# Performance work log

Measured on AMD Instinct MI355X. Metric: run time of the kernel, lower is better.

## Reference

```python
import jax, jax.numpy as jnp
import numpy as np

N_NODES = 100000
N_EDGES = 300000
D_IN = 256
D_OUT = 256
NEG_SLOPE = 0.2


def setup_inputs() -> dict:
    key = jax.random.key(0)
    ks = jax.random.split(key, 6)
    feat = jax.random.normal(ks[0], (N_NODES, D_IN), dtype=jnp.float32)
    # xavier-normal-ish init scale
    scale = (2.0 / (D_IN + D_OUT)) ** 0.5
    W_src = jax.random.normal(ks[1], (D_IN, D_OUT), dtype=jnp.float32) * scale
    b_src = jnp.zeros((D_OUT,), dtype=jnp.float32)
    W_dst = jax.random.normal(ks[2], (D_IN, D_OUT), dtype=jnp.float32) * scale
    b_dst = jnp.zeros((D_OUT,), dtype=jnp.float32)
    attn = jax.random.normal(ks[3], (D_OUT,), dtype=jnp.float32) * scale
    src = jax.random.randint(ks[4], (N_EDGES,), 0, N_NODES, dtype=jnp.int32)
    dst = jax.random.randint(ks[5], (N_EDGES,), 0, N_NODES, dtype=jnp.int32)
    return {"feat": feat, "W_src": W_src, "b_src": b_src,
            "W_dst": W_dst, "b_dst": b_dst, "attn": attn,
            "src": src, "dst": dst}


def reference(feat, W_src, b_src, W_dst, b_dst, attn, src, dst):
    N = feat.shape[0]
    # node projections (dense GEMMs)
    el = feat @ W_src + b_src          # [N, D_OUT]  (feat_src / 'el')
    er = feat @ W_dst + b_dst          # [N, D_OUT]  (feat_dst / 'er')
    # edge-wise u_add_v + LeakyReLU, then attention dot
    e = jax.nn.leaky_relu(el[src] + er[dst], NEG_SLOPE)  # [E, D_OUT]
    score = e @ attn                    # [E]  ((e*attn).sum(-1))
    # edge softmax segmented by destination node
    smax = jax.ops.segment_max(score, dst, num_segments=N)   # [N]
    ex = jnp.exp(score - smax[dst])                           # [E]
    ssum = jax.ops.segment_sum(ex, dst, num_segments=N)      # [N]
    a = ex / ssum[dst]                                        # [E]
    # weighted scatter-sum aggregation: u_mul_e('el','a') -> sum per dst
    out = jax.ops.segment_sum(el[src] * a[:, None], dst, num_segments=N)
    return out  # [N, D_OUT]
```

## Files before the change

kernel.cpp:

```cpp
#include <hip/hip_runtime.h>
#include <cstdint>
#include <cmath>

#define D 256
#define NEG 0.2f
#define BK 64

typedef __attribute__((ext_vector_type(8))) __bf16 bf16x8;
typedef __attribute__((ext_vector_type(8))) unsigned short ushort8;
typedef __attribute__((ext_vector_type(4))) float f32x4;

__device__ __forceinline__ unsigned short f2bf(float f){
    unsigned u = __float_as_uint(f);
    return (unsigned short)((u + 0x7fffu + ((u >> 16) & 1u)) >> 16);
}
__device__ __forceinline__ float b2f(unsigned short u){
    return __uint_as_float(((unsigned)u) << 16);
}

__device__ __forceinline__ void gload_lds16(const void* g, void* l){
    __builtin_amdgcn_global_load_lds(
        (const __attribute__((address_space(1))) unsigned int*)g,
        (__attribute__((address_space(3))) unsigned int*)l, 16, 0, 0);
}

__global__ __launch_bounds__(256) void prep_w_kernel(
    const float* __restrict__ Wsrc, const float* __restrict__ Wdst,
    const float* __restrict__ bsrc, const float* __restrict__ bdst,
    unsigned short* __restrict__ WT, float* __restrict__ biascat)
{
    int idx = blockIdx.x*256 + threadIdx.x;
    int col = idx >> 5;
    int u   = idx & 31;
    int gu  = (u & 24) | ((u ^ col) & 7);
    const float* W = (col < 256) ? Wsrc : Wdst;
    int c = col & 255;
    ushort8 o;
    #pragma unroll
    for (int j = 0; j < 8; ++j)
        o[j] = f2bf(W[(size_t)(gu*8 + j)*D + c]);
    *(ushort8*)(WT + (size_t)col*D + u*8) = o;
    if (idx < 512) biascat[idx] = (idx < 256) ? bsrc[idx] : bdst[idx-256];
}

__global__ __launch_bounds__(256) void prep_feat_kernel(
    const float* __restrict__ feat, unsigned short* __restrict__ featb, int N, int NPAD)
{
    int total = NPAD * 32;
    for (int idx = blockIdx.x*256 + threadIdx.x; idx < total; idx += gridDim.x*256){
        int r = idx >> 5;
        int u = idx & 31;
        ushort8 o;
        if (r < N){
            int gu = (u & 24) | ((u ^ r) & 7);
            const float* s = feat + (size_t)r*D + gu*8;
            float4 a = *(const float4*)s;
            float4 b = *(const float4*)(s + 4);
            o[0]=f2bf(a.x); o[1]=f2bf(a.y); o[2]=f2bf(a.z); o[3]=f2bf(a.w);
            o[4]=f2bf(b.x); o[5]=f2bf(b.y); o[6]=f2bf(b.z); o[7]=f2bf(b.w);
        } else {
            #pragma unroll
            for (int j = 0; j < 8; ++j) o[j] = 0;
        }
        *(ushort8*)(featb + (size_t)r*D + u*8) = o;
    }
}

__global__ __launch_bounds__(256) void proj_mfma_kernel(
    const unsigned short* __restrict__ featb, const unsigned short* __restrict__ WT,
    const float* __restrict__ biascat,
    unsigned short* __restrict__ el16, unsigned short* __restrict__ er16, int N)
{
    __shared__ unsigned short As[128*BK];
    __shared__ unsigned short Bs[128*BK];

    const int tid  = threadIdx.x;
    const int wave = tid >> 6;
    const int lane = tid & 63;
    const int col0 = blockIdx.x * 128;
    const int row0 = blockIdx.y * 128;
    const int wr = (wave >> 1) * 64;
    const int wc = (wave & 1) * 64;
    const int l15 = lane & 15;
    const int kg  = lane >> 4;

    const int sr = (wave << 3) + (lane >> 3);
    const int sc = (lane & 7) * 8;

    f32x4 acc[4][4] = {};

    for (int k0 = 0; k0 < D; k0 += BK) {
        #pragma unroll
        for (int r4 = 0; r4 < 4; ++r4) {
            int ar = r4*32 + sr;
            gload_lds16(featb + (size_t)(row0 + ar)*D + k0 + sc,
                        &As[(r4*32 + wave*8)*BK]);
            gload_lds16(WT + (size_t)(col0 + ar)*D + k0 + sc,
                        &Bs[(r4*32 + wave*8)*BK]);
        }
        __syncthreads();

        #pragma unroll
        for (int ks = 0; ks < 2; ++ks) {
            bf16x8 af[4], bfr[4];
            #pragma unroll
            for (int m = 0; m < 4; ++m){
                int row = wr + m*16 + l15;
                int c = ((kg + ks*4) ^ (row & 7)) * 8;
                af[m] = *(const bf16x8*)&As[row*BK + c];
            }
            #pragma unroll
            for (int n = 0; n < 4; ++n){
                int row = wc + n*16 + l15;
                int c = ((kg + ks*4) ^ (row & 7)) * 8;
                bfr[n] = *(const bf16x8*)&Bs[row*BK + c];
            }
            #pragma unroll
            for (int m = 0; m < 4; ++m)
                #pragma unroll
                for (int n = 0; n < 4; ++n)
                    acc[m][n] = __builtin_amdgcn_mfma_f32_16x16x32_bf16(bfr[n], af[m], acc[m][n], 0, 0, 0);
        }
        __syncthreads();
    }

    unsigned short* __restrict__ dstp = (col0 < 256) ? el16 : er16;
    const int ccbase = col0 & 255;
    #pragma unroll
    for (int m = 0; m < 4; ++m) {
        int row = row0 + wr + m*16 + l15;
        if (row >= N) continue;
        #pragma unroll
        for (int n = 0; n < 4; ++n) {
            int cw = wc + n*16 + kg*4;
            float4 b4 = *(const float4*)(biascat + col0 + cw);
            ushort4 o;
            o.x = f2bf(acc[m][n][0] + b4.x);
            o.y = f2bf(acc[m][n][1] + b4.y);
            o.z = f2bf(acc[m][n][2] + b4.z);
            o.w = f2bf(acc[m][n][3] + b4.w);
            *(ushort4*)(dstp + (size_t)row*D + ccbase + cw) = o;
        }
    }
}

__global__ void count_kernel(const int* __restrict__ dst, int* __restrict__ deg, int E){
    int e = blockIdx.x*blockDim.x + threadIdx.x;
    if (e < E) atomicAdd(&deg[dst[e]], 1);
}

__global__ __launch_bounds__(256) void scan1_kernel(const int* __restrict__ deg,
                                                    int* __restrict__ incl,
                                                    int* __restrict__ bsum, int N){
    __shared__ int s[256];
    int i = blockIdx.x*256 + threadIdx.x;
    int v = (i < N) ? deg[i] : 0;
    s[threadIdx.x] = v;
    __syncthreads();
    #pragma unroll
    for (int off = 1; off < 256; off <<= 1){
        int t = (threadIdx.x >= off) ? s[threadIdx.x - off] : 0;
        __syncthreads();
        s[threadIdx.x] += t;
        __syncthreads();
    }
    if (i < N) incl[i] = s[threadIdx.x];
    if (threadIdx.x == 255) bsum[blockIdx.x] = s[255];
}

__global__ __launch_bounds__(512) void scan2_kernel(int* __restrict__ bsum, int nb){
    __shared__ int s[512];
    int t = threadIdx.x;
    int v = (t < nb) ? bsum[t] : 0;
    s[t] = v;
    __syncthreads();
    #pragma unroll
    for (int off = 1; off < 512; off <<= 1){
        int u = (t >= off) ? s[t - off] : 0;
        __syncthreads();
        s[t] += u;
        __syncthreads();
    }
    if (t < nb) bsum[t] = s[t] - v;
}

__global__ __launch_bounds__(256) void scan3_kernel(const int* __restrict__ deg,
                                                    const int* __restrict__ incl,
                                                    const int* __restrict__ bsum,
                                                    int* __restrict__ rowstart,
                                                    int* __restrict__ cursor, int N){
    int i = blockIdx.x*256 + threadIdx.x;
    if (i < N){
        int st = incl[i] - deg[i] + bsum[blockIdx.x];
        rowstart[i] = st;
        cursor[i]   = st;
    }
}

__global__ void scatter_kernel(const int* __restrict__ dst, const int* __restrict__ src,
                               int* __restrict__ cursor, int* __restrict__ srcs, int E){
    int e = blockIdx.x*blockDim.x + threadIdx.x;
    if (e < E){
        int pos = atomicAdd(&cursor[dst[e]], 1);
        srcs[pos] = src[e];
    }
}

__global__ __launch_bounds__(256) void gat_node_kernel(
    const unsigned short* __restrict__ el16, const unsigned short* __restrict__ er16,
    const float* __restrict__ attn, const int* __restrict__ srcs,
    const int* __restrict__ rowstart, const int* __restrict__ degv,
    float* __restrict__ out, int N)
{
    int node = blockIdx.x*4 + (threadIdx.x >> 6);
    if (node >= N) return;
    int lane = threadIdx.x & 63;
    float4 o = make_float4(0.f,0.f,0.f,0.f);
    int deg = degv[node];
    float* op = out + (size_t)node*D + lane*4;
    if (deg == 0){ *(float4*)op = o; return; }

    ushort4 rv = *(const ushort4*)(er16 + (size_t)node*D + lane*4);
    float4 r4 = make_float4(b2f(rv.x), b2f(rv.y), b2f(rv.z), b2f(rv.w));
    float4 a4 = *(const float4*)(attn + lane*4);
    int start = rowstart[node];

    float m = -INFINITY, ssum = 0.f;
    for (int base = 0; base < deg; base += 4){
        int cnt = deg - base; if (cnt > 4) cnt = 4;
        float4 l[4]; float p[4];
        #pragma unroll
        for (int j = 0; j < 4; ++j){
            int k = base + j; if (k >= deg) k = deg - 1;
            int sn = srcs[start + k];
            ushort4 lv = *(const ushort4*)(el16 + (size_t)sn*D + lane*4);
            l[j] = make_float4(b2f(lv.x), b2f(lv.y), b2f(lv.z), b2f(lv.w));
        }
        #pragma unroll
        for (int j = 0; j < 4; ++j){
            float x, pp = 0.f;
            x = l[j].x + r4.x; pp += (x > 0.f ? x : NEG*x) * a4.x;
            x = l[j].y + r4.y; pp += (x > 0.f ? x : NEG*x) * a4.y;
            x = l[j].z + r4.z; pp += (x > 0.f ? x : NEG*x) * a4.z;
            x = l[j].w + r4.w; pp += (x > 0.f ? x : NEG*x) * a4.w;
            p[j] = pp;
        }
        #pragma unroll
        for (int off = 32; off > 0; off >>= 1){
            #pragma unroll
            for (int j = 0; j < 4; ++j) p[j] += __shfl_xor(p[j], off, 64);
        }
        #pragma unroll
        for (int j = 0; j < 4; ++j){
            if (j >= cnt) break;
            float newm  = fmaxf(m, p[j]);
            float scale = __expf(m - newm);
            float w     = __expf(p[j] - newm);
            ssum = ssum*scale + w;
            o.x = o.x*scale + w*l[j].x;
            o.y = o.y*scale + w*l[j].y;
            o.z = o.z*scale + w*l[j].z;
            o.w = o.w*scale + w*l[j].w;
            m = newm;
        }
    }
    float inv = 1.f/ssum;
    o.x *= inv; o.y *= inv; o.z *= inv; o.w *= inv;
    *(float4*)op = o;
}

extern "C" void kernel_launch(void* const* d_in, const int* in_sizes, int n_in,
                              void* d_out, int out_size, void* d_ws, size_t ws_size,
                              hipStream_t stream)
{
    const float* feat = (const float*)d_in[0];
    const float* Wsrc = (const float*)d_in[1];
    const float* bsrc = (const float*)d_in[2];
    const float* Wdst = (const float*)d_in[3];
    const float* bdst = (const float*)d_in[4];
    const float* attn = (const float*)d_in[5];
    const int*   src  = (const int*)d_in[6];
    const int*   dst  = (const int*)d_in[7];
    const int N = in_sizes[0] / D;
    const int E = in_sizes[6];
    const int NPAD = ((N + 127)/128)*128;
    float* out = (float*)d_out;

    unsigned short* el16 = (unsigned short*)d_ws;
    unsigned short* er16 = el16 + (size_t)N*D;
    int* deg      = (int*)(er16 + (size_t)N*D);
    int* incl     = deg + N;
    int* rowstart = incl + N;
    int* cursor   = rowstart + N;
    int* bsum     = cursor + N;
    int* srcs     = bsum + 512;
    unsigned short* WT = (unsigned short*)(srcs + E);
    float* biascat = (float*)(WT + (size_t)512*D);
    unsigned short* featb = (unsigned short*)(biascat + 512);

    const int nb = (N + 255)/256;

    hipMemsetAsync(deg, 0, (size_t)N*sizeof(int), stream);

    prep_w_kernel<<<64, 256, 0, stream>>>(Wsrc, Wdst, bsrc, bdst, WT, biascat);
    prep_feat_kernel<<<4096, 256, 0, stream>>>(feat, featb, N, NPAD);

    dim3 pgrid(4, NPAD/128);
    proj_mfma_kernel<<<pgrid, 256, 0, stream>>>(featb, WT, biascat, el16, er16, N);

    count_kernel<<<(E + 255)/256, 256, 0, stream>>>(dst, deg, E);
    scan1_kernel<<<nb, 256, 0, stream>>>(deg, incl, bsum, N);
    scan2_kernel<<<1, 512, 0, stream>>>(bsum, nb);
    scan3_kernel<<<nb, 256, 0, stream>>>(deg, incl, bsum, rowstart, cursor, N);
    scatter_kernel<<<(E + 255)/256, 256, 0, stream>>>(dst, src, cursor, srcs, E);

    gat_node_kernel<<<(N + 3)/4, 256, 0, stream>>>(el16, er16, attn, srcs,
                                                   rowstart, deg, out, N);
}
```

Baseline: 189.6 us.

## Double-buffer LDS tiles in projection GEMM and remap blocks for XCD locality

The projection GEMM kernel now double-buffers its A/B LDS tiles, prefetching the next K-slice with global_load_lds while computing the current one. It uses explicit vmcnt waits and raw barriers in place of __syncthreads. It also flattens the grid to 1D and remaps block IDs so the four column blocks of each row tile land on the same XCD, for better L2 reuse of feature rows. NPAD is rounded to 1024 to fit the mapping, which doubles LDS use and may lower occupancy.

```diff
diff --git a/kernel.cpp b/kernel.cpp
--- a/kernel.cpp
+++ b/kernel.cpp
@@ -5,6 +5,7 @@
 #define D 256
 #define NEG 0.2f
 #define BK 64
+#define NT (D/BK)
 
 typedef __attribute__((ext_vector_type(8))) __bf16 bf16x8;
 typedef __attribute__((ext_vector_type(8))) unsigned short ushort8;
@@ -71,14 +72,20 @@
     const float* __restrict__ biascat,
     unsigned short* __restrict__ el16, unsigned short* __restrict__ er16, int N)
 {
-    __shared__ unsigned short As[128*BK];
-    __shared__ unsigned short Bs[128*BK];
+    __shared__ unsigned short As[2][128*BK];
+    __shared__ unsigned short Bs[2][128*BK];
+
+    const int b    = blockIdx.x;
+    const int xcd  = b & 7;
+    const int s    = b >> 3;
+    const int p    = (s >> 2)*8 + xcd;
+    const int c    = s & 3;
+    const int row0 = p * 128;
+    const int col0 = c * 128;
 
     const int tid  = threadIdx.x;
     const int wave = tid >> 6;
     const int lane = tid & 63;
-    const int col0 = blockIdx.x * 128;
-    const int row0 = blockIdx.y * 128;
     const int wr = (wave >> 1) * 64;
     const int wc = (wave & 1) * 64;
     const int l15 = lane & 15;
@@ -89,16 +96,31 @@
 
     f32x4 acc[4][4] = {};
 
-    for (int k0 = 0; k0 < D; k0 += BK) {
-        #pragma unroll
-        for (int r4 = 0; r4 < 4; ++r4) {
-            int ar = r4*32 + sr;
-            gload_lds16(featb + (size_t)(row0 + ar)*D + k0 + sc,
-                        &As[(r4*32 + wave*8)*BK]);
-            gload_lds16(WT + (size_t)(col0 + ar)*D + k0 + sc,
-                        &Bs[(r4*32 + wave*8)*BK]);
-        }
-        __syncthreads();
+    #pragma unroll
+    for (int r4 = 0; r4 < 4; ++r4) {
+        int ar = r4*32 + sr;
+        gload_lds16(featb + (size_t)(row0 + ar)*D + 0 + sc, &As[0][(r4*32 + wave*8)*BK]);
+        gload_lds16(WT    + (size_t)(col0 + ar)*D + 0 + sc, &Bs[0][(r4*32 + wave*8)*BK]);
+    }
+
+    for (int t = 0; t < NT; ++t) {
+        const int cur = t & 1;
+        if (t + 1 < NT) {
+            int k0 = (t + 1) * BK;
+            #pragma unroll
+            for (int r4 = 0; r4 < 4; ++r4) {
+                int ar = r4*32 + sr;
+                gload_lds16(featb + (size_t)(row0 + ar)*D + k0 + sc,
+                            &As[cur ^ 1][(r4*32 + wave*8)*BK]);
+                gload_lds16(WT    + (size_t)(col0 + ar)*D + k0 + sc,
+                            &Bs[cur ^ 1][(r4*32 + wave*8)*BK]);
+            }
+            asm volatile("s_waitcnt vmcnt(8)" ::: "memory");
+        } else {
+            asm volatile("s_waitcnt vmcnt(0)" ::: "memory");
+        }
+        __builtin_amdgcn_s_barrier();
+        __builtin_amdgcn_sched_barrier(0);
 
         #pragma unroll
         for (int ks = 0; ks < 2; ++ks) {
@@ -106,14 +128,14 @@
             #pragma unroll
             for (int m = 0; m < 4; ++m){
                 int row = wr + m*16 + l15;
-                int c = ((kg + ks*4) ^ (row & 7)) * 8;
-                af[m] = *(const bf16x8*)&As[row*BK + c];
+                int cc = ((kg + ks*4) ^ (row & 7)) * 8;
+                af[m] = *(const bf16x8*)&As[cur][row*BK + cc];
             }
             #pragma unroll
             for (int n = 0; n < 4; ++n){
                 int row = wc + n*16 + l15;
-                int c = ((kg + ks*4) ^ (row & 7)) * 8;
-                bfr[n] = *(const bf16x8*)&Bs[row*BK + c];
+                int cc = ((kg + ks*4) ^ (row & 7)) * 8;
+                bfr[n] = *(const bf16x8*)&Bs[cur][row*BK + cc];
             }
             #pragma unroll
             for (int m = 0; m < 4; ++m)
@@ -121,7 +143,8 @@
                 for (int n = 0; n < 4; ++n)
                     acc[m][n] = __builtin_amdgcn_mfma_f32_16x16x32_bf16(bfr[n], af[m], acc[m][n], 0, 0, 0);
         }
-        __syncthreads();
+        __builtin_amdgcn_sched_barrier(0);
+        __builtin_amdgcn_s_barrier();
     }
 
     unsigned short* __restrict__ dstp = (col0 < 256) ? el16 : er16;
@@ -283,7 +306,8 @@
     const int*   dst  = (const int*)d_in[7];
     const int N = in_sizes[0] / D;
     const int E = in_sizes[6];
-    const int NPAD = ((N + 127)/128)*128;
+    const int NPAD = ((N + 1023)/1024)*1024;
+    const int NP = NPAD / 128;
     float* out = (float*)d_out;
 
     unsigned short* el16 = (unsigned short*)d_ws;
@@ -305,8 +329,7 @@
     prep_w_kernel<<<64, 256, 0, stream>>>(Wsrc, Wdst, bsrc, bdst, WT, biascat);
     prep_feat_kernel<<<4096, 256, 0, stream>>>(feat, featb, N, NPAD);
 
-    dim3 pgrid(4, NPAD/128);
-    proj_mfma_kernel<<<pgrid, 256, 0, stream>>>(featb, WT, biascat, el16, er16, N);
+    proj_mfma_kernel<<<4*NP, 256, 0, stream>>>(featb, WT, biascat, el16, er16, N);
 
     count_kernel<<<(E + 255)/256, 256, 0, stream>>>(dst, deg, E);
     scan1_kernel<<<nb, 256, 0, stream>>>(deg, incl, bsum, N);
```

New measurement: 186.9 us. No clear change (-1.4%).
